# Performance work log

Hardware: AMD Instinct MI355X
Metric: run time of the kernel (lower is better)

Reference implementation:

```python
import jax, jax.numpy as jnp
import numpy as np

# ---- static config (matches init_kwargs / input_specs) ----
MODEL_CONTEXT_LEN = 4096
BLOCK_SIZE = 16
NUM_Q_HEADS = 32
NUM_KV_HEADS = 8
HEAD_DIM = 128
ROPE_BASE = 10000.0
B = 8
NUM_PAST = 4613                                   # context_len - 1, same for all seqs
END_BNUM = NUM_PAST // BLOCK_SIZE                 # 288
REM = NUM_PAST % BLOCK_SIZE                       # 5
START_BNUM = (NUM_PAST - MODEL_CONTEXT_LEN) // BLOCK_SIZE + 2  # 34
CUR_POS = MODEL_CONTEXT_LEN - 1                   # 4095 (capped decode position)
BLOCKS_PER_SEQ = END_BNUM + 1                     # 289
NUM_BLOCKS = B * BLOCKS_PER_SEQ                   # 2312


def rope(pos, x):
    """NeoX-style rotary. pos: [T] int; x: [..., T, H, D]."""
    half = HEAD_DIM // 2
    inv = 1.0 / (ROPE_BASE ** (jnp.arange(half, dtype=jnp.float32) / half))
    freqs = pos.astype(jnp.float32)[:, None] * inv        # [T, half]
    cos = jnp.cos(freqs)[:, None, :]                      # [T, 1, half]
    sin = jnp.sin(freqs)[:, None, :]
    x1, x2 = jnp.split(x, 2, axis=-1)
    return jnp.concatenate([x1 * cos - x2 * sin, x2 * cos + x1 * sin], axis=-1)


def setup_inputs() -> dict:
    key = jax.random.key(0)
    ks = jax.random.split(key, 7)
    q = jax.random.normal(ks[0], (B, NUM_Q_HEADS * HEAD_DIM), jnp.float32)
    k = jax.random.normal(ks[1], (B, NUM_KV_HEADS * HEAD_DIM), jnp.float32)
    v = jax.random.normal(ks[2], (B, NUM_KV_HEADS * HEAD_DIM), jnp.float32)
    positions = jnp.full((B,), NUM_PAST, dtype=jnp.int32)
    context_lens = jnp.full((B,), NUM_PAST + 1, dtype=jnp.int32)
    # distinct physical blocks per sequence (paged layout)
    block_tables = jnp.arange(NUM_BLOCKS, dtype=jnp.int32).reshape(B, BLOCKS_PER_SEQ)
    # cache stores UN-rotated keys (module writes k_original); layout [nblk, bs, Hk, D]
    key_cache = jax.random.normal(ks[3], (NUM_BLOCKS, BLOCK_SIZE, NUM_KV_HEADS, HEAD_DIM), jnp.float32) * 0.5
    value_cache = jax.random.normal(ks[4], (NUM_BLOCKS, BLOCK_SIZE, NUM_KV_HEADS, HEAD_DIM), jnp.float32) * 0.5
    W_o = jax.random.normal(ks[5], (NUM_Q_HEADS * HEAD_DIM, NUM_Q_HEADS * HEAD_DIM), jnp.float32) * 0.02
    return {"q": q, "k": k, "v": v, "positions": positions, "context_lens": context_lens,
            "block_tables": block_tables, "key_cache": key_cache, "value_cache": value_cache, "W_o": W_o}


def reference(q, k, v, positions, context_lens, block_tables, key_cache, value_cache, W_o):
    # Decode path of StreamingAttentionSink, context > model_context_len:
    # gather sink block + sliding-window blocks, re-apply rotary at shifted
    # positions, attend with q/k roped at capped position, project output.
    # positions for re-roped past keys: sink tokens 0..bs-1, window tokens
    # 2*bs-1-rem .. model_context_len-2 (matches the torch code's pos arange).
    pos_sink = np.arange(BLOCK_SIZE)
    pos_win = np.arange(2 * BLOCK_SIZE - 1 - REM, MODEL_CONTEXT_LEN - 1)
    POS = jnp.asarray(np.concatenate([pos_sink, pos_win]), dtype=jnp.int32)  # [4085]

    qh = q.reshape(B, NUM_Q_HEADS, HEAD_DIM)
    kh = k.reshape(B, NUM_KV_HEADS, HEAD_DIM)
    vh = v.reshape(B, NUM_KV_HEADS, HEAD_DIM)

    # phys_bnums = [block_table[0]] + block_table[start:end]  -> [B, 255]
    phys = jnp.concatenate([block_tables[:, :1], block_tables[:, START_BNUM:END_BNUM]], axis=1)
    full_k = key_cache[phys].reshape(B, -1, NUM_KV_HEADS, HEAD_DIM)       # [B, 4080, Hk, D]
    rem_k = key_cache[block_tables[:, END_BNUM], :REM]                     # [B, 5, Hk, D]
    past_k = jnp.concatenate([full_k, rem_k], axis=1)                      # [B, 4085, Hk, D]
    full_v = value_cache[phys].reshape(B, -1, NUM_KV_HEADS, HEAD_DIM)
    rem_v = value_cache[block_tables[:, END_BNUM], :REM]
    past_v = jnp.concatenate([full_v, rem_v], axis=1)

    past_k = rope(POS, past_k)  # re-apply rotary to shifted sink/window keys

    cur = jnp.array([CUR_POS], dtype=jnp.int32)
    q_rot = rope(cur, qh[:, None, :, :])[:, 0]   # [B, H, D] at capped position
    k_rot = rope(cur, kh[:, None, :, :])[:, 0]   # [B, Hk, D]

    keys = jnp.concatenate([past_k, k_rot[:, None]], axis=1)   # [B, 4086, Hk, D]
    vals = jnp.concatenate([past_v, vh[:, None]], axis=1)

    # GQA attention (group = 4 q-heads per kv-head)
    G = NUM_Q_HEADS // NUM_KV_HEADS
    qg = q_rot.reshape(B, NUM_KV_HEADS, G, HEAD_DIM)
    scale = 1.0 / np.sqrt(HEAD_DIM).astype(np.float32)
    scores = jnp.einsum('bhgd,bthd->bhgt', qg, keys) * scale
    probs = jax.nn.softmax(scores, axis=-1)
    attn = jnp.einsum('bhgt,bthd->bhgd', probs, vals).reshape(B, NUM_Q_HEADS * HEAD_DIM)
    return attn @ W_o
```

## Files before the change

kernel.cpp:

```cpp
#include <hip/hip_runtime.h>
#include <math.h>

#define NB 8
#define NQH 32
#define NKVH 8
#define HD 128
#define GQ 4
#define T_TOT 4086
#define SPLITS 16
#define TCHUNK 256
#define TILE 32
#define PAD 132
#define BPS 289
#define LOG2_10K_OVER_64 0.2076205059304601f
#define SCALE 0.08838834764831843f

#define PART_ATTN_OFF 0
#define PART_ATTN_SZ  (64 * GQ * SPLITS * PAD)
#define ATTN_OFF      (PART_ATTN_OFF + PART_ATTN_SZ)
#define ATTN_SZ       (NB * 4096)
#define PART_GEMM_OFF (ATTN_OFF + ATTN_SZ)
#define PART_GEMM_SZ  (16 * 32768)

__global__ __launch_bounds__(256) void attn_partial_kernel(
    const float* __restrict__ q, const float* __restrict__ k, const float* __restrict__ v,
    const int* __restrict__ bt, const float* __restrict__ kc, const float* __restrict__ vc,
    float* __restrict__ part)
{
    __shared__ float kt[TILE][PAD];
    __shared__ float vt[TILE][PAD];
    __shared__ float qs[GQ][HD];
    __shared__ float sc[GQ][TILE];
    __shared__ float inv_s[64];
    __shared__ int   ptile[TILE];

    const int tid  = threadIdx.x;
    const int bh   = blockIdx.x;
    const int s    = blockIdx.y;
    const int b    = bh >> 3, h = bh & 7;
    const int lane = tid & 63, wave = tid >> 6;

    if (tid < 64) inv_s[tid] = exp2f(-(float)tid * LOG2_10K_OVER_64);
    __syncthreads();

    const float* qp = q + (size_t)b * (NQH * HD) + (size_t)h * (GQ * HD);
    for (int e = tid; e < GQ * HD; e += 256) {
        int g = e >> 7, d = e & 127, j = d & 63;
        float freq = 4095.0f * inv_s[j];
        float sn, cs; sincosf(freq, &sn, &cs);
        float x1 = qp[g * HD + j], x2 = qp[g * HD + j + 64];
        qs[g][d] = (d < 64) ? (x1 * cs - x2 * sn) : (x2 * cs + x1 * sn);
    }

    float m_run = -INFINITY, l_run = 0.0f, acc_lo = 0.0f, acc_hi = 0.0f;
    const int t0 = s * TCHUNK;
    const int* btb = bt + b * BPS;

    for (int tb = 0; tb < TCHUNK; tb += TILE) {
        __syncthreads();

        for (int e = tid; e < TILE * 32; e += 256) {
            int row = e >> 5, c4 = (e & 31) << 2;
            int tg = t0 + tb + row;
            if (tg <= T_TOT - 1) {
                const float *ksrc, *vsrc; int pos;
                if (tg == T_TOT - 1) {
                    ksrc = k + (size_t)(b * NKVH + h) * HD;
                    vsrc = v + (size_t)(b * NKVH + h) * HD;
                    pos = 4095;
                } else {
                    int bti, rr;
                    if (tg < 16)        { bti = 0;              rr = tg;        pos = tg;      }
                    else if (tg < 4080) { bti = 33 + (tg >> 4); rr = tg & 15;   pos = tg + 10; }
                    else                { bti = 288;            rr = tg - 4080; pos = tg + 10; }
                    int blk = btb[bti];
                    size_t off = (((size_t)blk * 16 + rr) * NKVH + h) * HD;
                    ksrc = kc + off; vsrc = vc + off;
                }
                float4 kk = *(const float4*)(ksrc + c4);
                float4 vv = *(const float4*)(vsrc + c4);
                *(float4*)&kt[row][c4] = kk;
                *(float4*)&vt[row][c4] = vv;
                if ((e & 31) == 0) ptile[row] = pos;
            } else {
                float4 z = {0.f, 0.f, 0.f, 0.f};
                *(float4*)&kt[row][c4] = z;
                *(float4*)&vt[row][c4] = z;
                if ((e & 31) == 0) ptile[row] = 0;
            }
        }
        __syncthreads();

        for (int e = tid; e < TILE * 64; e += 256) {
            int row = e >> 6, j = e & 63;
            float freq = (float)ptile[row] * inv_s[j];
            float sn, cs; sincosf(freq, &sn, &cs);
            float x1 = kt[row][j], x2 = kt[row][j + 64];
            kt[row][j]      = x1 * cs - x2 * sn;
            kt[row][j + 64] = x2 * cs + x1 * sn;
        }
        __syncthreads();

        if (tid < 128) {
            int t = tid & 31, g = tid >> 5;
            int tg = t0 + tb + t;
            float dot = 0.f;
            #pragma unroll
            for (int d4 = 0; d4 < 32; ++d4) {
                float4 kk = *(const float4*)&kt[t][d4 << 2];
                float4 qq = *(const float4*)&qs[g][d4 << 2];
                dot += kk.x * qq.x + kk.y * qq.y + kk.z * qq.z + kk.w * qq.w;
            }
            sc[g][t] = (tg <= T_TOT - 1) ? dot * SCALE : -INFINITY;
        }
        __syncthreads();

        {
            int g = wave;
            int tl = lane & 31;
            float sv = sc[g][tl];
            float mx = sv;
            #pragma unroll
            for (int off = 16; off; off >>= 1) mx = fmaxf(mx, __shfl_xor(mx, off));
            float m_new = fmaxf(m_run, mx);
            float alpha = expf(m_run - m_new);
            float p = expf(sv - m_new);
            float ps = p;
            #pragma unroll
            for (int off = 16; off; off >>= 1) ps += __shfl_xor(ps, off);
            l_run = l_run * alpha + ps;
            m_run = m_new;
            acc_lo *= alpha; acc_hi *= alpha;
            if (lane < 32) sc[g][tl] = p;
            #pragma unroll 8
            for (int t = 0; t < TILE; ++t) {
                float pv = sc[g][t];
                acc_lo += pv * vt[t][lane];
                acc_hi += pv * vt[t][lane + 64];
            }
        }
    }

    float* pp = part + ((size_t)(bh * GQ + wave) * SPLITS + s) * PAD;
    pp[lane] = acc_lo;
    pp[lane + 64] = acc_hi;
    if (lane == 0) { pp[128] = m_run; pp[129] = l_run; }
}

__global__ __launch_bounds__(256) void attn_reduce_kernel(
    const float* __restrict__ part, float* __restrict__ attn)
{
    int bh = blockIdx.x;
    int tid = threadIdx.x;
    int g = tid >> 6, lane = tid & 63;
    const float* pg = part + (size_t)(bh * GQ + g) * SPLITS * PAD;
    float mstar = -INFINITY;
    #pragma unroll
    for (int s = 0; s < SPLITS; ++s) mstar = fmaxf(mstar, pg[s * PAD + 128]);
    float accl = 0.f, acch = 0.f, l = 0.f;
    #pragma unroll
    for (int s = 0; s < SPLITS; ++s) {
        float w = expf(pg[s * PAD + 128] - mstar);
        l    += pg[s * PAD + 129] * w;
        accl += w * pg[s * PAD + lane];
        acch += w * pg[s * PAD + lane + 64];
    }
    int b = bh >> 3, h = bh & 7;
    float inv_l = 1.0f / l;
    size_t base = (size_t)b * 4096 + (size_t)(h * GQ + g) * 128;
    attn[base + lane]      = accl * inv_l;
    attn[base + lane + 64] = acch * inv_l;
}

__global__ __launch_bounds__(256) void gemm_partial_kernel(
    const float* __restrict__ attn, const float* __restrict__ Wo,
    float* __restrict__ part)
{
    __shared__ float a_s[NB][256];
    int tid = threadIdx.x;
    int jt = blockIdx.x & 15, is = blockIdx.x >> 4;
    int i0 = is * 256;
    int c  = jt * 256 + tid;
    for (int e = tid; e < NB * 256; e += 256) {
        int bb = e >> 8, i = e & 255;
        a_s[bb][i] = attn[(size_t)bb * 4096 + i0 + i];
    }
    __syncthreads();
    float acc[NB] = {0.f, 0.f, 0.f, 0.f, 0.f, 0.f, 0.f, 0.f};
    #pragma unroll 4
    for (int i = 0; i < 256; ++i) {
        float w = Wo[(size_t)(i0 + i) * 4096 + c];
        #pragma unroll
        for (int bb = 0; bb < NB; ++bb) acc[bb] += a_s[bb][i] * w;
    }
    for (int bb = 0; bb < NB; ++bb)
        part[(size_t)is * 32768 + (size_t)bb * 4096 + c] = acc[bb];
}

__global__ __launch_bounds__(256) void gemm_reduce_kernel(
    const float* __restrict__ part, float* __restrict__ out)
{
    int idx = blockIdx.x * 256 + threadIdx.x;
    float4 sum = {0.f, 0.f, 0.f, 0.f};
    #pragma unroll
    for (int s = 0; s < 16; ++s) {
        float4 p = *(const float4*)(part + (size_t)s * 32768 + (size_t)idx * 4);
        sum.x += p.x; sum.y += p.y; sum.z += p.z; sum.w += p.w;
    }
    *(float4*)(out + (size_t)idx * 4) = sum;
}

extern "C" void kernel_launch(void* const* d_in, const int* in_sizes, int n_in,
                              void* d_out, int out_size, void* d_ws, size_t ws_size,
                              hipStream_t stream) {
    const float* q  = (const float*)d_in[0];
    const float* k  = (const float*)d_in[1];
    const float* v  = (const float*)d_in[2];
    const int*   bt = (const int*)d_in[5];
    const float* kc = (const float*)d_in[6];
    const float* vc = (const float*)d_in[7];
    const float* Wo = (const float*)d_in[8];
    float* out = (float*)d_out;
    float* ws  = (float*)d_ws;

    float* part_attn = ws + PART_ATTN_OFF;
    float* attn      = ws + ATTN_OFF;
    float* part_gemm = ws + PART_GEMM_OFF;

    attn_partial_kernel<<<dim3(64, SPLITS), 256, 0, stream>>>(q, k, v, bt, kc, vc, part_attn);
    attn_reduce_kernel<<<64, 256, 0, stream>>>(part_attn, attn);
    gemm_partial_kernel<<<256, 256, 0, stream>>>(attn, Wo, part_gemm);
    gemm_reduce_kernel<<<32, 256, 0, stream>>>(part_gemm, out);
}
```

Before: 397.0 us.

## Rework attention partials with fused rope, max-free softmax, and retiled output GEMM

Doubles the sequence splits and precomputes per-token cache offsets and positions in shared memory. Applies rotary during the key load, using hardware sin/cos with manual range reduction. Drops the running-max softmax rescaling: probabilities are plain exponentials of pre-scaled scores, and the split reduce becomes a simple sum. Spreads the score and PV work across all waves. The output GEMM is retiled to float2 columns, with a per-wave K split reduced in shared memory. This removes sincos, expf and sync overhead, at the risk of exp overflow for large scores.

Measured after the change: 360.9 us. 1.1x faster.

```diff
diff --git a/kernel.cpp b/kernel.cpp
--- a/kernel.cpp
+++ b/kernel.cpp
@@ -7,144 +7,160 @@
 #define HD 128
 #define GQ 4
 #define T_TOT 4086
-#define SPLITS 16
-#define TCHUNK 256
+#define SPLITS 32
+#define TCHUNK 128
 #define TILE 32
-#define PAD 132
+#define PPAD 130
 #define BPS 289
 #define LOG2_10K_OVER_64 0.2076205059304601f
 #define SCALE 0.08838834764831843f
 
 #define PART_ATTN_OFF 0
-#define PART_ATTN_SZ  (64 * GQ * SPLITS * PAD)
-#define ATTN_OFF      (PART_ATTN_OFF + PART_ATTN_SZ)
-#define ATTN_SZ       (NB * 4096)
-#define PART_GEMM_OFF (ATTN_OFF + ATTN_SZ)
-#define PART_GEMM_SZ  (16 * 32768)
+#define PART_ATTN_SZ  (64 * GQ * SPLITS * PPAD)
+#define ATTN_OFF      PART_ATTN_SZ
+#define PART_GEMM_OFF 0
+
+__device__ __forceinline__ void rope_cs(float posf, int j, float& cs, float& sn)
+{
+    const float INV2PI = 0.15915494309189535f;
+    const float P1 = 6.28125f;
+    const float P2 = 0.0019354820251464844f;
+    const float P3 = -1.748455600075e-7f;
+    float inv  = __builtin_amdgcn_exp2f(-(float)j * LOG2_10K_OVER_64);
+    float freq = posf * inv;
+    float n    = rintf(freq * INV2PI);
+    float red  = fmaf(-n, P1, freq);
+    red        = fmaf(-n, P2, red);
+    red        = fmaf(-n, P3, red);
+    float rev  = red * INV2PI;
+    sn = __builtin_amdgcn_sinf(rev);
+    cs = __builtin_amdgcn_cosf(rev);
+}
 
 __global__ __launch_bounds__(256) void attn_partial_kernel(
     const float* __restrict__ q, const float* __restrict__ k, const float* __restrict__ v,
     const int* __restrict__ bt, const float* __restrict__ kc, const float* __restrict__ vc,
     float* __restrict__ part)
 {
-    __shared__ float kt[TILE][PAD];
-    __shared__ float vt[TILE][PAD];
-    __shared__ float qs[GQ][HD];
-    __shared__ float sc[GQ][TILE];
-    __shared__ float inv_s[64];
-    __shared__ int   ptile[TILE];
+    __shared__ float kt[TILE][132];
+    __shared__ float vt[TILE][128];
+    __shared__ float qs[GQ][132];
+    __shared__ float sc[GQ][36];
+    __shared__ unsigned int offr[TCHUNK];
+    __shared__ int posr[TCHUNK];
+    __shared__ float lred[4][GQ];
 
     const int tid  = threadIdx.x;
     const int bh   = blockIdx.x;
     const int s    = blockIdx.y;
     const int b    = bh >> 3, h = bh & 7;
-    const int lane = tid & 63, wave = tid >> 6;
-
-    if (tid < 64) inv_s[tid] = exp2f(-(float)tid * LOG2_10K_OVER_64);
-    __syncthreads();
-
-    const float* qp = q + (size_t)b * (NQH * HD) + (size_t)h * (GQ * HD);
-    for (int e = tid; e < GQ * HD; e += 256) {
-        int g = e >> 7, d = e & 127, j = d & 63;
-        float freq = 4095.0f * inv_s[j];
-        float sn, cs; sincosf(freq, &sn, &cs);
-        float x1 = qp[g * HD + j], x2 = qp[g * HD + j + 64];
-        qs[g][d] = (d < 64) ? (x1 * cs - x2 * sn) : (x2 * cs + x1 * sn);
-    }
-
-    float m_run = -INFINITY, l_run = 0.0f, acc_lo = 0.0f, acc_hi = 0.0f;
-    const int t0 = s * TCHUNK;
+    const int lane = tid & 63, w = tid >> 6;
+    const int t0   = s * TCHUNK;
     const int* btb = bt + b * BPS;
+
+    if (tid < TCHUNK) {
+        int tg = t0 + tid;
+        unsigned int off; int pos;
+        if (tg == T_TOT - 1)      { off = 0xFFFFFFFFu; pos = 4095; }
+        else if (tg < T_TOT - 1) {
+            int bti, rr;
+            if (tg < 16)        { bti = 0;              rr = tg;        pos = tg;      }
+            else if (tg < 4080) { bti = 33 + (tg >> 4); rr = tg & 15;   pos = tg + 10; }
+            else                { bti = 288;            rr = tg - 4080; pos = tg + 10; }
+            off = (unsigned int)(((btb[bti] * 16 + rr) * NKVH + h) * HD);
+        } else                    { off = 0u; pos = 0; }
+        offr[tid] = off; posr[tid] = pos;
+    }
+    {
+        const float* qp = q + (size_t)b * (NQH * HD) + (size_t)h * (GQ * HD);
+        for (int e = tid; e < GQ * HD; e += 256) {
+            int g = e >> 7, d = e & 127, j = d & 63;
+            float cs, sn; rope_cs(4095.0f, j, cs, sn);
+            float x1 = qp[g * HD + j], x2 = qp[g * HD + j + 64];
+            qs[g][d] = ((d < 64) ? (x1 * cs - x2 * sn) : (x2 * cs + x1 * sn)) * SCALE;
+        }
+    }
+
+    float acc0 = 0.f, acc1 = 0.f, l_run = 0.f;
+    const int g_s = (lane >> 4) & 3, tl_s = (lane >> 1) & 7, hf = lane & 1;
+    const int gp = w >> 1, cc = (w & 1) * 64 + lane;
 
     for (int tb = 0; tb < TCHUNK; tb += TILE) {
         __syncthreads();
 
-        for (int e = tid; e < TILE * 32; e += 256) {
+        #pragma unroll
+        for (int it = 0; it < 2; ++it) {
+            int e = tid + it * 256;
+            int row = e >> 4, c4 = (e & 15) << 2;
+            unsigned int off = offr[tb + row];
+            float posf = (float)posr[tb + row];
+            const float* ks = (off == 0xFFFFFFFFu) ? (k + (size_t)(b * NKVH + h) * HD)
+                                                   : (kc + off);
+            float4 k1 = *(const float4*)(ks + c4);
+            float4 k2 = *(const float4*)(ks + 64 + c4);
+            float4 lo, hi; float cs, sn;
+            rope_cs(posf, c4 + 0, cs, sn); lo.x = k1.x*cs - k2.x*sn; hi.x = k2.x*cs + k1.x*sn;
+            rope_cs(posf, c4 + 1, cs, sn); lo.y = k1.y*cs - k2.y*sn; hi.y = k2.y*cs + k1.y*sn;
+            rope_cs(posf, c4 + 2, cs, sn); lo.z = k1.z*cs - k2.z*sn; hi.z = k2.z*cs + k1.z*sn;
+            rope_cs(posf, c4 + 3, cs, sn); lo.w = k1.w*cs - k2.w*sn; hi.w = k2.w*cs + k1.w*sn;
+            *(float4*)&kt[row][c4]      = lo;
+            *(float4*)&kt[row][64 + c4] = hi;
+        }
+        #pragma unroll
+        for (int it = 0; it < 4; ++it) {
+            int e = tid + it * 256;
             int row = e >> 5, c4 = (e & 31) << 2;
-            int tg = t0 + tb + row;
-            if (tg <= T_TOT - 1) {
-                const float *ksrc, *vsrc; int pos;
-                if (tg == T_TOT - 1) {
-                    ksrc = k + (size_t)(b * NKVH + h) * HD;
-                    vsrc = v + (size_t)(b * NKVH + h) * HD;
-                    pos = 4095;
-                } else {
-                    int bti, rr;
-                    if (tg < 16)        { bti = 0;              rr = tg;        pos = tg;      }
-                    else if (tg < 4080) { bti = 33 + (tg >> 4); rr = tg & 15;   pos = tg + 10; }
-                    else                { bti = 288;            rr = tg - 4080; pos = tg + 10; }
-                    int blk = btb[bti];
-                    size_t off = (((size_t)blk * 16 + rr) * NKVH + h) * HD;
-                    ksrc = kc + off; vsrc = vc + off;
-                }
-                float4 kk = *(const float4*)(ksrc + c4);
-                float4 vv = *(const float4*)(vsrc + c4);
-                *(float4*)&kt[row][c4] = kk;
-                *(float4*)&vt[row][c4] = vv;
-                if ((e & 31) == 0) ptile[row] = pos;
-            } else {
-                float4 z = {0.f, 0.f, 0.f, 0.f};
-                *(float4*)&kt[row][c4] = z;
-                *(float4*)&vt[row][c4] = z;
-                if ((e & 31) == 0) ptile[row] = 0;
-            }
+            unsigned int off = offr[tb + row];
+            const float* vs = (off == 0xFFFFFFFFu) ? (v + (size_t)(b * NKVH + h) * HD)
+                                                   : (vc + off);
+            *(float4*)&vt[row][c4] = *(const float4*)(vs + c4);
         }
         __syncthreads();
 
-        for (int e = tid; e < TILE * 64; e += 256) {
-            int row = e >> 6, j = e & 63;
-            float freq = (float)ptile[row] * inv_s[j];
-            float sn, cs; sincosf(freq, &sn, &cs);
-            float x1 = kt[row][j], x2 = kt[row][j + 64];
-            kt[row][j]      = x1 * cs - x2 * sn;
-            kt[row][j + 64] = x2 * cs + x1 * sn;
-        }
-        __syncthreads();
-
-        if (tid < 128) {
-            int t = tid & 31, g = tid >> 5;
-            int tg = t0 + tb + t;
+        {
+            int t = w * 8 + tl_s;
+            const float* kr = &kt[t][hf * 64];
+            const float* qr = &qs[g_s][hf * 64];
             float dot = 0.f;
             #pragma unroll
-            for (int d4 = 0; d4 < 32; ++d4) {
-                float4 kk = *(const float4*)&kt[t][d4 << 2];
-                float4 qq = *(const float4*)&qs[g][d4 << 2];
-                dot += kk.x * qq.x + kk.y * qq.y + kk.z * qq.z + kk.w * qq.w;
+            for (int j4 = 0; j4 < 16; ++j4) {
+                float4 kk = *(const float4*)(kr + (j4 << 2));
+                float4 qq = *(const float4*)(qr + (j4 << 2));
+                dot += kk.x*qq.x + kk.y*qq.y + kk.z*qq.z + kk.w*qq.w;
             }
-            sc[g][t] = (tg <= T_TOT - 1) ? dot * SCALE : -INFINITY;
+            dot += __shfl_xor(dot, 1);
+            int tg = t0 + tb + t;
+            float p = (tg < T_TOT) ? __builtin_amdgcn_exp2f(dot * 1.4426950408889634f) : 0.f;
+            l_run += p;
+            if (hf == 0) sc[g_s][t] = p;
         }
         __syncthreads();
 
-        {
-            int g = wave;
-            int tl = lane & 31;
-            float sv = sc[g][tl];
-            float mx = sv;
-            #pragma unroll
-            for (int off = 16; off; off >>= 1) mx = fmaxf(mx, __shfl_xor(mx, off));
-            float m_new = fmaxf(m_run, mx);
-            float alpha = expf(m_run - m_new);
-            float p = expf(sv - m_new);
-            float ps = p;
-            #pragma unroll
-            for (int off = 16; off; off >>= 1) ps += __shfl_xor(ps, off);
-            l_run = l_run * alpha + ps;
-            m_run = m_new;
-            acc_lo *= alpha; acc_hi *= alpha;
-            if (lane < 32) sc[g][tl] = p;
-            #pragma unroll 8
-            for (int t = 0; t < TILE; ++t) {
-                float pv = sc[g][t];
-                acc_lo += pv * vt[t][lane];
-                acc_hi += pv * vt[t][lane + 64];
-            }
-        }
-    }
-
-    float* pp = part + ((size_t)(bh * GQ + wave) * SPLITS + s) * PAD;
-    pp[lane] = acc_lo;
-    pp[lane + 64] = acc_hi;
-    if (lane == 0) { pp[128] = m_run; pp[129] = l_run; }
+        #pragma unroll
+        for (int t4 = 0; t4 < 8; ++t4) {
+            float4 p40 = *(const float4*)&sc[2*gp][t4 << 2];
+            float4 p41 = *(const float4*)&sc[2*gp + 1][t4 << 2];
+            int t = t4 << 2;
+            float v0 = vt[t][cc], v1 = vt[t+1][cc], v2 = vt[t+2][cc], v3 = vt[t+3][cc];
+            acc0 += p40.x*v0 + p40.y*v1 + p40.z*v2 + p40.w*v3;
+            acc1 += p41.x*v0 + p41.y*v1 + p41.z*v2 + p41.w*v3;
+        }
+    }
+
+    float lr = l_run;
+    lr += __shfl_xor(lr, 1); lr += __shfl_xor(lr, 2);
+    lr += __shfl_xor(lr, 4); lr += __shfl_xor(lr, 8);
+    if ((lane & 15) == 0) lred[w][lane >> 4] = lr;
+    __syncthreads();
+
+    float* pp0 = part + ((size_t)(bh * GQ + 2*gp    ) * SPLITS + s) * PPAD;
+    float* pp1 = part + ((size_t)(bh * GQ + 2*gp + 1) * SPLITS + s) * PPAD;
+    pp0[cc] = acc0;
+    pp1[cc] = acc1;
+    if (tid < GQ) {
+        float l = 0.5f * (lred[0][tid] + lred[1][tid] + lred[2][tid] + lred[3][tid]);
+        part[((size_t)(bh * GQ + tid) * SPLITS + s) * PPAD + 129] = l;
+    }
 }
 
 __global__ __launch_bounds__(256) void attn_reduce_kernel(
@@ -153,17 +169,13 @@
     int bh = blockIdx.x;
     int tid = threadIdx.x;
     int g = tid >> 6, lane = tid & 63;
-    const float* pg = part + (size_t)(bh * GQ + g) * SPLITS * PAD;
-    float mstar = -INFINITY;
-    #pragma unroll
-    for (int s = 0; s < SPLITS; ++s) mstar = fmaxf(mstar, pg[s * PAD + 128]);
+    const float* pg = part + (size_t)(bh * GQ + g) * SPLITS * PPAD;
     float accl = 0.f, acch = 0.f, l = 0.f;
-    #pragma unroll
+    #pragma unroll 8
     for (int s = 0; s < SPLITS; ++s) {
-        float w = expf(pg[s * PAD + 128] - mstar);
-        l    += pg[s * PAD + 129] * w;
-        accl += w * pg[s * PAD + lane];
-        acch += w * pg[s * PAD + lane + 64];
+        l    += pg[s * PPAD + 129];
+        accl += pg[s * PPAD + lane];
+        acch += pg[s * PPAD + lane + 64];
     }
     int b = bh >> 3, h = bh & 7;
     float inv_l = 1.0f / l;
@@ -177,24 +189,42 @@
     float* __restrict__ part)
 {
     __shared__ float a_s[NB][256];
+    __shared__ float red[4][NB][128];
     int tid = threadIdx.x;
-    int jt = blockIdx.x & 15, is = blockIdx.x >> 4;
+    int lane = tid & 63, w = tid >> 6;
+    int jt = blockIdx.x;
+    int is = blockIdx.y;
     int i0 = is * 256;
-    int c  = jt * 256 + tid;
+    int c  = jt * 128 + lane * 2;
     for (int e = tid; e < NB * 256; e += 256) {
         int bb = e >> 8, i = e & 255;
         a_s[bb][i] = attn[(size_t)bb * 4096 + i0 + i];
     }
     __syncthreads();
-    float acc[NB] = {0.f, 0.f, 0.f, 0.f, 0.f, 0.f, 0.f, 0.f};
-    #pragma unroll 4
-    for (int i = 0; i < 256; ++i) {
-        float w = Wo[(size_t)(i0 + i) * 4096 + c];
-        #pragma unroll
-        for (int bb = 0; bb < NB; ++bb) acc[bb] += a_s[bb][i] * w;
-    }
-    for (int bb = 0; bb < NB; ++bb)
-        part[(size_t)is * 32768 + (size_t)bb * 4096 + c] = acc[bb];
+    float accx[NB] = {}, accy[NB] = {};
+    const float* wp = Wo + (size_t)(i0 + w * 64) * 4096 + c;
+    #pragma unroll 8
+    for (int ii = 0; ii < 64; ++ii) {
+        float2 wv = *(const float2*)(wp + (size_t)ii * 4096);
+        int il = w * 64 + ii;
+        #pragma unroll
+        for (int bb = 0; bb < NB; ++bb) {
+            float a = a_s[bb][il];
+            accx[bb] += a * wv.x;
+            accy[bb] += a * wv.y;
+        }
+    }
+    #pragma unroll
+    for (int bb = 0; bb < NB; ++bb) {
+        red[w][bb][lane * 2]     = accx[bb];
+        red[w][bb][lane * 2 + 1] = accy[bb];
+    }
+    __syncthreads();
+    for (int e = tid; e < NB * 128; e += 256) {
+        int bb = e >> 7, l = e & 127;
+        float sum = red[0][bb][l] + red[1][bb][l] + red[2][bb][l] + red[3][bb][l];
+        part[(size_t)is * 32768 + (size_t)bb * 4096 + jt * 128 + l] = sum;
+    }
 }
 
 __global__ __launch_bounds__(256) void gemm_reduce_kernel(
@@ -229,6 +259,6 @@
 
     attn_partial_kernel<<<dim3(64, SPLITS), 256, 0, stream>>>(q, k, v, bt, kc, vc, part_attn);
     attn_reduce_kernel<<<64, 256, 0, stream>>>(part_attn, attn);
-    gemm_partial_kernel<<<256, 256, 0, stream>>>(attn, Wo, part_gemm);
+    gemm_partial_kernel<<<dim3(32, 16), 256, 0, stream>>>(attn, Wo, part_gemm);
     gemm_reduce_kernel<<<32, 256, 0, stream>>>(part_gemm, out);
 }
```
